# Kernel optimization log

Measured on AMD Instinct MI355X. Metric: run time of the kernel, lower is better.

The kernel has to match this reference:

```python
import jax, jax.numpy as jnp
import numpy as np

B, S, D = 32, 1, 2048
H, KVH, HD = 16, 4, 128
MAXS = 4096
EPS = 1e-5
NREP = H // KVH  # GQA repeat factor = 4
FF = 4 * D
POS = 4095  # decode position (start_pos)


def setup_inputs() -> dict:
    key = jax.random.key(0)
    ks = jax.random.split(key, 12)
    sc = lambda d: 1.0 / np.sqrt(d)
    # RoPE angles for the current token position, [S, HD//2]
    inv_freq = 1.0 / (10000.0 ** (np.arange(0, HD, 2, dtype=np.float32) / HD))
    ang = (POS + np.arange(S, dtype=np.float32))[:, None] * inv_freq[None, :]
    return {
        "x": jax.random.normal(ks[0], (B, S, D), jnp.float32),
        "cos": jnp.asarray(np.cos(ang), jnp.float32),
        "sin": jnp.asarray(np.sin(ang), jnp.float32),
        "k_cache": jax.random.normal(ks[1], (B, MAXS, KVH, HD), jnp.float32),
        "v_cache": jax.random.normal(ks[2], (B, MAXS, KVH, HD), jnp.float32),
        "w_rms_attn": jnp.ones((D,), jnp.float32),
        "wq": jax.random.normal(ks[3], (D, D), jnp.float32) * sc(D),
        "wk": jax.random.normal(ks[4], (D, KVH * HD), jnp.float32) * sc(D),
        "wv": jax.random.normal(ks[5], (D, KVH * HD), jnp.float32) * sc(D),
        "wo": jax.random.normal(ks[6], (D, D), jnp.float32) * sc(D),
        "w_rms_ffn": jnp.ones((D,), jnp.float32),
        "w1": jax.random.normal(ks[7], (D, FF), jnp.float32) * sc(D),
        "w2": jax.random.normal(ks[8], (D, FF), jnp.float32) * sc(D),
        "w3": jax.random.normal(ks[9], (FF, D), jnp.float32) * sc(FF),
        "start_pos": POS,
    }


def _rmsnorm(x, g):
    return x * g * jax.lax.rsqrt(jnp.mean(x * x, axis=-1, keepdims=True) + EPS)


def _rope(x, cos, sin):
    # x: [B, S, h, HD]; complex rotation on (even, odd) pairs
    xr = x.reshape(*x.shape[:-1], HD // 2, 2)
    x0, x1 = xr[..., 0], xr[..., 1]
    c = cos[None, :, None, :]
    s = sin[None, :, None, :]
    r0 = x0 * c - x1 * s
    r1 = x0 * s + x1 * c
    return jnp.stack([r0, r1], axis=-1).reshape(x.shape)


def reference(x, cos, sin, k_cache, v_cache, w_rms_attn, wq, wk, wv, wo,
              w_rms_ffn, w1, w2, w3, start_pos):
    xa = _rmsnorm(x, w_rms_attn)
    xq = (xa @ wq).reshape(B, S, H, HD)
    xk = (xa @ wk).reshape(B, S, KVH, HD)
    xv = (xa @ wv).reshape(B, S, KVH, HD)
    # Source applies RoPE to K and V (not Q) -- reproduced faithfully.
    xk = _rope(xk, cos, sin)
    xv = _rope(xv, cos, sin)
    kc = jax.lax.dynamic_update_slice(k_cache, xk, (0, start_pos, 0, 0))
    vc = jax.lax.dynamic_update_slice(v_cache, xv, (0, start_pos, 0, 0))
    klen = start_pos + S
    keys = jnp.repeat(kc[:, :klen], NREP, axis=2)   # [B, klen, H, HD]
    vals = jnp.repeat(vc[:, :klen], NREP, axis=2)
    att = jnp.einsum('bqhd,bkhd->bhqk', xq, keys) * (HD ** -0.5)
    att = jax.nn.softmax(att, axis=-1)
    y = jnp.einsum('bhqk,bkhd->bqhd', att, vals).reshape(B, S, D)
    h = x + y @ wo
    xf = _rmsnorm(h, w_rms_ffn)
    return h + (jax.nn.silu(xf @ w1) * (xf @ w2)) @ w3
```

## Files before the change

kernel.cpp:

```cpp
#include <hip/hip_runtime.h>
#include <math.h>

#define BB 32
#define DD 2048
#define NKVH 4
#define HDIM 128
#define MAXS 4096
#define FFD 8192
#define POS 4095
#define EPSV 1e-5f
#define SCALE 0.08838834764831845f
#define ASPLIT 16

#define OFF_QT   0u
#define OFF_KT   65536u
#define OFF_VT   81920u
#define OFF_G1   98304u
#define OFF_G2   360448u
#define ZERO_N   622592u
#define OFF_XAT  622592u
#define OFF_RK   688128u
#define OFF_RV   704512u
#define OFF_PML  720896u
#define OFF_PACC 737280u
#define OFF_YT   1785856u
#define OFF_H    1851392u
#define OFF_XFT  1916928u

#define REP32(M) M(0) M(1) M(2) M(3) M(4) M(5) M(6) M(7) M(8) M(9) M(10) M(11) M(12) M(13) M(14) M(15) M(16) M(17) M(18) M(19) M(20) M(21) M(22) M(23) M(24) M(25) M(26) M(27) M(28) M(29) M(30) M(31)
#define REP32A(M,X) M(0,X) M(1,X) M(2,X) M(3,X) M(4,X) M(5,X) M(6,X) M(7,X) M(8,X) M(9,X) M(10,X) M(11,X) M(12,X) M(13,X) M(14,X) M(15,X) M(16,X) M(17,X) M(18,X) M(19,X) M(20,X) M(21,X) M(22,X) M(23,X) M(24,X) M(25,X) M(26,X) M(27,X) M(28,X) M(29,X) M(30,X) M(31,X)

#define DECLA(i) float a##i = 0.f;
#define FMA1(i,k) a##i = fmaf(ap[(k)*32 + (i)], w##k, a##i);
#define STORET(i) tl[i] = a##i;
#define ATOMN(i) atomicAdd(C + (size_t)(i)*N + n, a##i);

template<int N, int CH, bool TOUT>
__device__ __forceinline__ void gemv_body(const float* __restrict__ At,
                                          const float* __restrict__ W,
                                          float* __restrict__ C, int colblk,
                                          float* tile) {
    int tid = (int)threadIdx.x;
    int n = colblk * 256 + tid;
    int d0 = blockIdx.y * CH;
    const float* Wp = W + (size_t)d0 * N + n;
    const float* ap = At + (size_t)d0 * 32;
    REP32(DECLA)
#pragma unroll 4
    for (int dd = 0; dd < CH; dd += 4) {
        float w0 = Wp[0];
        float w1 = Wp[(size_t)N];
        float w2 = Wp[(size_t)N * 2];
        float w3 = Wp[(size_t)N * 3];
        REP32A(FMA1, 0)
        REP32A(FMA1, 1)
        REP32A(FMA1, 2)
        REP32A(FMA1, 3)
        Wp += (size_t)N * 4;
        ap += 128;
    }
    if constexpr (TOUT) {
        float* tl = tile + tid * 33;
        REP32(STORET)
        __syncthreads();
        float* cb = C + (size_t)colblk * 256 * 32;
#pragma unroll
        for (int i = 0; i < 32; ++i) {
            int f = i * 256 + tid;
            atomicAdd(cb + f, tile[(f >> 5) * 33 + (f & 31)]);
        }
    } else {
        REP32(ATOMN)
    }
}

template<int N, int CH, bool TOUT>
__global__ __launch_bounds__(256) void gemv32_kernel(const float* __restrict__ At,
                                                     const float* __restrict__ W,
                                                     float* __restrict__ C) {
    if constexpr (TOUT) {
        __shared__ float tile[256 * 33];
        gemv_body<N, CH, true>(At, W, C, blockIdx.x, tile);
    } else {
        gemv_body<N, CH, false>(At, W, C, blockIdx.x, nullptr);
    }
}

template<int N, int CH, int HALF>
__global__ __launch_bounds__(256) void gemv32_dual_kernel(const float* __restrict__ At,
        const float* __restrict__ W0, const float* __restrict__ W1,
        float* __restrict__ C0, float* __restrict__ C1) {
    __shared__ float tile[256 * 33];
    int bx = blockIdx.x;
    if (bx < HALF) gemv_body<N, CH, true>(At, W0, C0, bx, tile);
    else           gemv_body<N, CH, true>(At, W1, C1, bx - HALF, tile);
}

__global__ void zero_kernel(float* __restrict__ p) {
    p[blockIdx.x * 256 + threadIdx.x] = 0.f;
}

__global__ void rmsnorm_kernel(const float* __restrict__ in, const float* __restrict__ g,
                               float* __restrict__ outT, float* __restrict__ cpy) {
    int b = blockIdx.x;
    int tid = threadIdx.x;
    const float* row = in + b * DD;
    float v[8];
    float ss = 0.f;
#pragma unroll
    for (int i = 0; i < 8; ++i) { v[i] = row[tid + i * 256]; ss += v[i] * v[i]; }
#pragma unroll
    for (int off = 32; off; off >>= 1) ss += __shfl_xor(ss, off);
    __shared__ float red[4];
    if ((tid & 63) == 0) red[tid >> 6] = ss;
    __syncthreads();
    ss = red[0] + red[1] + red[2] + red[3];
    float scale = rsqrtf(ss * (1.f / DD) + EPSV);
#pragma unroll
    for (int i = 0; i < 8; ++i) {
        int idx = tid + i * 256;
        outT[(size_t)idx * 32 + b] = v[i] * g[idx] * scale;
        if (cpy) cpy[b * DD + idx] = v[i];
    }
}

__global__ void rope_kernel(const float* __restrict__ kT, const float* __restrict__ vT,
                            const float* __restrict__ cosb, const float* __restrict__ sinb,
                            float* __restrict__ rk, float* __restrict__ rv) {
    int idx = blockIdx.x * 256 + threadIdx.x;
    int b = idx >> 8, rem = idx & 255;
    int kvh = rem >> 6, i = rem & 63;
    float c = cosb[i], s = sinb[i];
    int col = kvh * HDIM + 2 * i;
    float k0 = kT[(size_t)col * 32 + b], k1 = kT[(size_t)(col + 1) * 32 + b];
    float v0 = vT[(size_t)col * 32 + b], v1 = vT[(size_t)(col + 1) * 32 + b];
    int o = (b * NKVH + kvh) * HDIM + 2 * i;
    rk[o] = k0 * c - k1 * s; rk[o + 1] = k0 * s + k1 * c;
    rv[o] = v0 * c - v1 * s; rv[o + 1] = v0 * s + v1 * c;
}

__global__ __launch_bounds__(256) void attn_partial_kernel(
    const float* __restrict__ qT, const float* __restrict__ kc, const float* __restrict__ vc,
    const float* __restrict__ rk, const float* __restrict__ rv,
    float* __restrict__ pml, float* __restrict__ pacc) {
    int bid = blockIdx.x;
    int split = bid & 15, kvh = (bid >> 4) & 3, b = bid >> 6;
    int tid = threadIdx.x;
    __shared__ float q_s[4][HDIM];
    __shared__ float p_s[4][256];
    __shared__ float red[8][4][HDIM];
    for (int i = tid; i < 4 * HDIM; i += 256)
        q_s[i >> 7][i & 127] = qT[(size_t)(kvh * 512 + i) * 32 + b];
    __syncthreads();
    int t0 = split * 256;
    {
        int t = t0 + tid;
        const float* krow = (t == POS) ? rk + (b * NKVH + kvh) * HDIM
                                       : kc + ((size_t)(b * MAXS + t) * NKVH + kvh) * HDIM;
        float s0 = 0, s1 = 0, s2 = 0, s3 = 0;
#pragma unroll 8
        for (int j = 0; j < HDIM; j += 4) {
            float4 kk = *(const float4*)(krow + j);
            s0 += kk.x * q_s[0][j] + kk.y * q_s[0][j + 1] + kk.z * q_s[0][j + 2] + kk.w * q_s[0][j + 3];
            s1 += kk.x * q_s[1][j] + kk.y * q_s[1][j + 1] + kk.z * q_s[1][j + 2] + kk.w * q_s[1][j + 3];
            s2 += kk.x * q_s[2][j] + kk.y * q_s[2][j + 1] + kk.z * q_s[2][j + 2] + kk.w * q_s[2][j + 3];
            s3 += kk.x * q_s[3][j] + kk.y * q_s[3][j + 1] + kk.z * q_s[3][j + 2] + kk.w * q_s[3][j + 3];
        }
        p_s[0][tid] = s0 * SCALE; p_s[1][tid] = s1 * SCALE;
        p_s[2][tid] = s2 * SCALE; p_s[3][tid] = s3 * SCALE;
    }
    __syncthreads();
    {
        int w = tid >> 6, lane = tid & 63;
        float e0 = p_s[w][lane], e1 = p_s[w][lane + 64];
        float e2 = p_s[w][lane + 128], e3 = p_s[w][lane + 192];
        float m = fmaxf(fmaxf(e0, e1), fmaxf(e2, e3));
#pragma unroll
        for (int off = 32; off; off >>= 1) m = fmaxf(m, __shfl_xor(m, off));
        e0 = __expf(e0 - m); e1 = __expf(e1 - m);
        e2 = __expf(e2 - m); e3 = __expf(e3 - m);
        p_s[w][lane] = e0; p_s[w][lane + 64] = e1;
        p_s[w][lane + 128] = e2; p_s[w][lane + 192] = e3;
        float l = e0 + e1 + e2 + e3;
#pragma unroll
        for (int off = 32; off; off >>= 1) l += __shfl_xor(l, off);
        if (lane == 0) {
            int idx = ((b * NKVH + kvh) * ASPLIT + split) * 4 + w;
            pml[2 * idx] = m; pml[2 * idx + 1] = l;
        }
    }
    __syncthreads();
    {
        int tsub = tid >> 5, q4 = tid & 31;
        int tb = t0 + tsub * 32;
        const float* vbase = vc + ((size_t)(b * MAXS + tb) * NKVH + kvh) * HDIM + q4 * 4;
        float4 a0 = {0, 0, 0, 0}, a1 = a0, a2 = a0, a3 = a0;
        int jmax = (split == ASPLIT - 1 && tsub == 7) ? 31 : 32;
#pragma unroll 4
        for (int j = 0; j < jmax; ++j) {
            float4 vv = *(const float4*)(vbase + (size_t)j * (NKVH * HDIM));
            int tl = tsub * 32 + j;
            float p0 = p_s[0][tl], p1 = p_s[1][tl], p2 = p_s[2][tl], p3 = p_s[3][tl];
            a0.x = fmaf(p0, vv.x, a0.x); a0.y = fmaf(p0, vv.y, a0.y); a0.z = fmaf(p0, vv.z, a0.z); a0.w = fmaf(p0, vv.w, a0.w);
            a1.x = fmaf(p1, vv.x, a1.x); a1.y = fmaf(p1, vv.y, a1.y); a1.z = fmaf(p1, vv.z, a1.z); a1.w = fmaf(p1, vv.w, a1.w);
            a2.x = fmaf(p2, vv.x, a2.x); a2.y = fmaf(p2, vv.y, a2.y); a2.z = fmaf(p2, vv.z, a2.z); a2.w = fmaf(p2, vv.w, a2.w);
            a3.x = fmaf(p3, vv.x, a3.x); a3.y = fmaf(p3, vv.y, a3.y); a3.z = fmaf(p3, vv.z, a3.z); a3.w = fmaf(p3, vv.w, a3.w);
        }
        if (split == ASPLIT - 1 && tsub == 7) {
            float4 vv = *(const float4*)(rv + (b * NKVH + kvh) * HDIM + q4 * 4);
            float p0 = p_s[0][255], p1 = p_s[1][255], p2 = p_s[2][255], p3 = p_s[3][255];
            a0.x = fmaf(p0, vv.x, a0.x); a0.y = fmaf(p0, vv.y, a0.y); a0.z = fmaf(p0, vv.z, a0.z); a0.w = fmaf(p0, vv.w, a0.w);
            a1.x = fmaf(p1, vv.x, a1.x); a1.y = fmaf(p1, vv.y, a1.y); a1.z = fmaf(p1, vv.z, a1.z); a1.w = fmaf(p1, vv.w, a1.w);
            a2.x = fmaf(p2, vv.x, a2.x); a2.y = fmaf(p2, vv.y, a2.y); a2.z = fmaf(p2, vv.z, a2.z); a2.w = fmaf(p2, vv.w, a2.w);
            a3.x = fmaf(p3, vv.x, a3.x); a3.y = fmaf(p3, vv.y, a3.y); a3.z = fmaf(p3, vv.z, a3.z); a3.w = fmaf(p3, vv.w, a3.w);
        }
        *(float4*)&red[tsub][0][q4 * 4] = a0;
        *(float4*)&red[tsub][1][q4 * 4] = a1;
        *(float4*)&red[tsub][2][q4 * 4] = a2;
        *(float4*)&red[tsub][3][q4 * 4] = a3;
    }
    __syncthreads();
    if (tid < 128) {
        int h = tid >> 5, qq = tid & 31;
        float4 s = {0, 0, 0, 0};
#pragma unroll
        for (int r = 0; r < 8; ++r) {
            float4 t4 = *(const float4*)&red[r][h][qq * 4];
            s.x += t4.x; s.y += t4.y; s.z += t4.z; s.w += t4.w;
        }
        int idx = ((b * NKVH + kvh) * ASPLIT + split) * 4 + h;
        *(float4*)(pacc + (size_t)idx * HDIM + qq * 4) = s;
    }
}

__global__ void attn_combine_kernel(const float* __restrict__ pml,
                                    const float* __restrict__ pacc, float* __restrict__ yT) {
    int bid = blockIdx.x;
    int b = bid >> 4, h = bid & 15;
    int kvh = h >> 2, hl = h & 3;
    int d = threadIdx.x;
    float M = -INFINITY;
#pragma unroll
    for (int s = 0; s < ASPLIT; ++s) {
        int idx = ((b * NKVH + kvh) * ASPLIT + s) * 4 + hl;
        M = fmaxf(M, pml[2 * idx]);
    }
    float denom = 0.f, acc = 0.f;
#pragma unroll
    for (int s = 0; s < ASPLIT; ++s) {
        int idx = ((b * NKVH + kvh) * ASPLIT + s) * 4 + hl;
        float e = __expf(pml[2 * idx] - M);
        denom += pml[2 * idx + 1] * e;
        acc += e * pacc[(size_t)idx * HDIM + d];
    }
    yT[(size_t)(h * HDIM + d) * 32 + b] = acc / denom;
}

__global__ void silu_mul_kernel(float* __restrict__ g1, const float* __restrict__ g2) {
    int i = blockIdx.x * 256 + threadIdx.x;
    float a = g1[i], bb = g2[i];
    g1[i] = a * bb / (1.f + __expf(-a));
}

extern "C" void kernel_launch(void* const* d_in, const int* in_sizes, int n_in,
                              void* d_out, int out_size, void* d_ws, size_t ws_size,
                              hipStream_t stream) {
    (void)in_sizes; (void)n_in; (void)out_size; (void)ws_size;
    const float* x    = (const float*)d_in[0];
    const float* cosb = (const float*)d_in[1];
    const float* sinb = (const float*)d_in[2];
    const float* kc   = (const float*)d_in[3];
    const float* vc   = (const float*)d_in[4];
    const float* wra  = (const float*)d_in[5];
    const float* wq   = (const float*)d_in[6];
    const float* wk   = (const float*)d_in[7];
    const float* wv   = (const float*)d_in[8];
    const float* wo   = (const float*)d_in[9];
    const float* wrf  = (const float*)d_in[10];
    const float* w1   = (const float*)d_in[11];
    const float* w2   = (const float*)d_in[12];
    const float* w3   = (const float*)d_in[13];
    float* out = (float*)d_out;
    float* ws  = (float*)d_ws;

    float* qT   = ws + OFF_QT;
    float* kT   = ws + OFF_KT;
    float* vT   = ws + OFF_VT;
    float* g1T  = ws + OFF_G1;
    float* g2T  = ws + OFF_G2;
    float* xaT  = ws + OFF_XAT;
    float* rk   = ws + OFF_RK;
    float* rv   = ws + OFF_RV;
    float* pml  = ws + OFF_PML;
    float* pacc = ws + OFF_PACC;
    float* yT   = ws + OFF_YT;
    float* h    = ws + OFF_H;
    float* xfT  = ws + OFF_XFT;

    zero_kernel<<<ZERO_N / 256, 256, 0, stream>>>(ws);

    rmsnorm_kernel<<<32, 256, 0, stream>>>(x, wra, xaT, h);
    gemv32_kernel<2048, 32, true><<<dim3(8, 64), 256, 0, stream>>>(xaT, wq, qT);
    gemv32_dual_kernel<512, 32, 2><<<dim3(4, 64), 256, 0, stream>>>(xaT, wk, wv, kT, vT);
    rope_kernel<<<32, 256, 0, stream>>>(kT, vT, cosb, sinb, rk, rv);
    attn_partial_kernel<<<2048, 256, 0, stream>>>(qT, kc, vc, rk, rv, pml, pacc);
    attn_combine_kernel<<<512, 128, 0, stream>>>(pml, pacc, yT);
    gemv32_kernel<2048, 32, false><<<dim3(8, 64), 256, 0, stream>>>(yT, wo, h);
    rmsnorm_kernel<<<32, 256, 0, stream>>>(h, wrf, xfT, out);
    gemv32_dual_kernel<8192, 128, 32><<<dim3(64, 16), 256, 0, stream>>>(xfT, w1, w2, g1T, g2T);
    silu_mul_kernel<<<1024, 256, 0, stream>>>(g1T, g2T);
    gemv32_kernel<2048, 128, false><<<dim3(8, 64), 256, 0, stream>>>(g1T, w3, out);
}
```

Baseline: 296.7 us.

## Restructure attention partial so each block covers all KV heads with coalesced rows

The attention partial kernel now assigns one block per (batch, 128-position split) covering all four KV heads. Each thread holds a float4 slice of the query in registers and reads contiguous 4 KB K/V rows, so the whole wavefront issues fully coalesced loads instead of per-thread strided row walks. QK dot products are reduced with cross-lane shuffles, and the partial-result layout and combine kernel are reindexed for 32 splits. The cost is five shuffle rounds per position and a larger partial buffer to combine.

```diff
diff --git a/kernel.cpp b/kernel.cpp
--- a/kernel.cpp
+++ b/kernel.cpp
@@ -10,7 +10,8 @@
 #define POS 4095
 #define EPSV 1e-5f
 #define SCALE 0.08838834764831845f
-#define ASPLIT 16
+#define ASPLIT 32
+#define SPOS 128
 
 #define OFF_QT   0u
 #define OFF_KT   65536u
@@ -22,10 +23,10 @@
 #define OFF_RK   688128u
 #define OFF_RV   704512u
 #define OFF_PML  720896u
-#define OFF_PACC 737280u
-#define OFF_YT   1785856u
-#define OFF_H    1851392u
-#define OFF_XFT  1916928u
+#define OFF_PACC 753664u
+#define OFF_YT   2850816u
+#define OFF_H    2916352u
+#define OFF_XFT  2981888u
 
 #define REP32(M) M(0) M(1) M(2) M(3) M(4) M(5) M(6) M(7) M(8) M(9) M(10) M(11) M(12) M(13) M(14) M(15) M(16) M(17) M(18) M(19) M(20) M(21) M(22) M(23) M(24) M(25) M(26) M(27) M(28) M(29) M(30) M(31)
 #define REP32A(M,X) M(0,X) M(1,X) M(2,X) M(3,X) M(4,X) M(5,X) M(6,X) M(7,X) M(8,X) M(9,X) M(10,X) M(11,X) M(12,X) M(13,X) M(14,X) M(15,X) M(16,X) M(17,X) M(18,X) M(19,X) M(20,X) M(21,X) M(22,X) M(23,X) M(24,X) M(25,X) M(26,X) M(27,X) M(28,X) M(29,X) M(30,X) M(31,X)
@@ -144,92 +145,125 @@
     const float* __restrict__ rk, const float* __restrict__ rv,
     float* __restrict__ pml, float* __restrict__ pacc) {
     int bid = blockIdx.x;
-    int split = bid & 15, kvh = (bid >> 4) & 3, b = bid >> 6;
+    int split = bid & 31, b = bid >> 5;
     int tid = threadIdx.x;
-    __shared__ float q_s[4][HDIM];
-    __shared__ float p_s[4][256];
-    __shared__ float red[8][4][HDIM];
-    for (int i = tid; i < 4 * HDIM; i += 256)
-        q_s[i >> 7][i & 127] = qT[(size_t)(kvh * 512 + i) * 32 + b];
+    int kvh = (tid >> 5) & 3;
+    int c = tid & 31;
+    int hi = tid >> 7;
+    __shared__ float p_s[16][SPOS];
+    __shared__ float red[128][17];
+
+    float4 q4[4];
+#pragma unroll
+    for (int h = 0; h < 4; ++h) {
+        int col = (kvh * 4 + h) * HDIM + c * 4;
+        q4[h].x = qT[(size_t)(col + 0) * 32 + b];
+        q4[h].y = qT[(size_t)(col + 1) * 32 + b];
+        q4[h].z = qT[(size_t)(col + 2) * 32 + b];
+        q4[h].w = qT[(size_t)(col + 3) * 32 + b];
+    }
+    int t0 = split * SPOS;
+    const float* kbase = kc + (size_t)(b * MAXS + t0) * (NKVH * HDIM);
+    const float* vbase = vc + (size_t)(b * MAXS + t0) * (NKVH * HDIM);
+
+#define QK_BODY(SRC, POSL)                                                      \
+    {                                                                           \
+        float4 kk = *(const float4*)(SRC);                                      \
+        float r0 = kk.x * q4[0].x + kk.y * q4[0].y + kk.z * q4[0].z + kk.w * q4[0].w; \
+        float r1 = kk.x * q4[1].x + kk.y * q4[1].y + kk.z * q4[1].z + kk.w * q4[1].w; \
+        float r2 = kk.x * q4[2].x + kk.y * q4[2].y + kk.z * q4[2].z + kk.w * q4[2].w; \
+        float r3 = kk.x * q4[3].x + kk.y * q4[3].y + kk.z * q4[3].z + kk.w * q4[3].w; \
+        _Pragma("unroll")                                                       \
+        for (int m = 1; m < 32; m <<= 1) {                                      \
+            r0 += __shfl_xor(r0, m); r1 += __shfl_xor(r1, m);                   \
+            r2 += __shfl_xor(r2, m); r3 += __shfl_xor(r3, m);                   \
+        }                                                                       \
+        if (c == 0) {                                                           \
+            p_s[kvh * 4 + 0][POSL] = r0 * SCALE;                                \
+            p_s[kvh * 4 + 1][POSL] = r1 * SCALE;                                \
+            p_s[kvh * 4 + 2][POSL] = r2 * SCALE;                                \
+            p_s[kvh * 4 + 3][POSL] = r3 * SCALE;                                \
+        }                                                                       \
+    }
+
+#pragma unroll 8
+    for (int iter = 0; iter < 63; ++iter) {
+        QK_BODY(kbase + iter * 1024 + tid * 4, iter * 2 + hi)
+    }
+    {
+        int posl = 126 + hi;
+        const float* src = (t0 + posl == POS)
+            ? rk + (size_t)(b * NKVH + kvh) * HDIM + c * 4
+            : kbase + 63 * 1024 + tid * 4;
+        QK_BODY(src, posl)
+    }
     __syncthreads();
-    int t0 = split * 256;
-    {
-        int t = t0 + tid;
-        const float* krow = (t == POS) ? rk + (b * NKVH + kvh) * HDIM
-                                       : kc + ((size_t)(b * MAXS + t) * NKVH + kvh) * HDIM;
-        float s0 = 0, s1 = 0, s2 = 0, s3 = 0;
-#pragma unroll 8
-        for (int j = 0; j < HDIM; j += 4) {
-            float4 kk = *(const float4*)(krow + j);
-            s0 += kk.x * q_s[0][j] + kk.y * q_s[0][j + 1] + kk.z * q_s[0][j + 2] + kk.w * q_s[0][j + 3];
-            s1 += kk.x * q_s[1][j] + kk.y * q_s[1][j + 1] + kk.z * q_s[1][j + 2] + kk.w * q_s[1][j + 3];
-            s2 += kk.x * q_s[2][j] + kk.y * q_s[2][j + 1] + kk.z * q_s[2][j + 2] + kk.w * q_s[2][j + 3];
-            s3 += kk.x * q_s[3][j] + kk.y * q_s[3][j + 1] + kk.z * q_s[3][j + 2] + kk.w * q_s[3][j + 3];
-        }
-        p_s[0][tid] = s0 * SCALE; p_s[1][tid] = s1 * SCALE;
-        p_s[2][tid] = s2 * SCALE; p_s[3][tid] = s3 * SCALE;
-    }
-    __syncthreads();
+
     {
         int w = tid >> 6, lane = tid & 63;
-        float e0 = p_s[w][lane], e1 = p_s[w][lane + 64];
-        float e2 = p_s[w][lane + 128], e3 = p_s[w][lane + 192];
-        float m = fmaxf(fmaxf(e0, e1), fmaxf(e2, e3));
-#pragma unroll
-        for (int off = 32; off; off >>= 1) m = fmaxf(m, __shfl_xor(m, off));
-        e0 = __expf(e0 - m); e1 = __expf(e1 - m);
-        e2 = __expf(e2 - m); e3 = __expf(e3 - m);
-        p_s[w][lane] = e0; p_s[w][lane + 64] = e1;
-        p_s[w][lane + 128] = e2; p_s[w][lane + 192] = e3;
-        float l = e0 + e1 + e2 + e3;
-#pragma unroll
-        for (int off = 32; off; off >>= 1) l += __shfl_xor(l, off);
-        if (lane == 0) {
-            int idx = ((b * NKVH + kvh) * ASPLIT + split) * 4 + w;
-            pml[2 * idx] = m; pml[2 * idx + 1] = l;
+#pragma unroll
+        for (int hh = 0; hh < 4; ++hh) {
+            int h = w * 4 + hh;
+            float e0 = p_s[h][lane], e1 = p_s[h][lane + 64];
+            float m = fmaxf(e0, e1);
+#pragma unroll
+            for (int off = 32; off; off >>= 1) m = fmaxf(m, __shfl_xor(m, off));
+            e0 = __expf(e0 - m); e1 = __expf(e1 - m);
+            p_s[h][lane] = e0; p_s[h][lane + 64] = e1;
+            float l = e0 + e1;
+#pragma unroll
+            for (int off = 32; off; off >>= 1) l += __shfl_xor(l, off);
+            if (lane == 0) {
+                int idx = ((b * ASPLIT + split) * 16 + h) * 2;
+                pml[idx] = m; pml[idx + 1] = l;
+            }
         }
     }
     __syncthreads();
+
+    float4 a0 = {0, 0, 0, 0}, a1 = a0, a2 = a0, a3 = a0;
+#define PV_BODY(SRC, POSL)                                                      \
+    {                                                                           \
+        float4 vv = *(const float4*)(SRC);                                      \
+        float p0 = p_s[kvh * 4 + 0][POSL], p1 = p_s[kvh * 4 + 1][POSL];         \
+        float p2 = p_s[kvh * 4 + 2][POSL], p3 = p_s[kvh * 4 + 3][POSL];         \
+        a0.x = fmaf(p0, vv.x, a0.x); a0.y = fmaf(p0, vv.y, a0.y);               \
+        a0.z = fmaf(p0, vv.z, a0.z); a0.w = fmaf(p0, vv.w, a0.w);               \
+        a1.x = fmaf(p1, vv.x, a1.x); a1.y = fmaf(p1, vv.y, a1.y);               \
+        a1.z = fmaf(p1, vv.z, a1.z); a1.w = fmaf(p1, vv.w, a1.w);               \
+        a2.x = fmaf(p2, vv.x, a2.x); a2.y = fmaf(p2, vv.y, a2.y);               \
+        a2.z = fmaf(p2, vv.z, a2.z); a2.w = fmaf(p2, vv.w, a2.w);               \
+        a3.x = fmaf(p3, vv.x, a3.x); a3.y = fmaf(p3, vv.y, a3.y);               \
+        a3.z = fmaf(p3, vv.z, a3.z); a3.w = fmaf(p3, vv.w, a3.w);               \
+    }
+#pragma unroll 8
+    for (int iter = 0; iter < 63; ++iter) {
+        PV_BODY(vbase + iter * 1024 + tid * 4, iter * 2 + hi)
+    }
     {
-        int tsub = tid >> 5, q4 = tid & 31;
-        int tb = t0 + tsub * 32;
-        const float* vbase = vc + ((size_t)(b * MAXS + tb) * NKVH + kvh) * HDIM + q4 * 4;
-        float4 a0 = {0, 0, 0, 0}, a1 = a0, a2 = a0, a3 = a0;
-        int jmax = (split == ASPLIT - 1 && tsub == 7) ? 31 : 32;
-#pragma unroll 4
-        for (int j = 0; j < jmax; ++j) {
-            float4 vv = *(const float4*)(vbase + (size_t)j * (NKVH * HDIM));
-            int tl = tsub * 32 + j;
-            float p0 = p_s[0][tl], p1 = p_s[1][tl], p2 = p_s[2][tl], p3 = p_s[3][tl];
-            a0.x = fmaf(p0, vv.x, a0.x); a0.y = fmaf(p0, vv.y, a0.y); a0.z = fmaf(p0, vv.z, a0.z); a0.w = fmaf(p0, vv.w, a0.w);
-            a1.x = fmaf(p1, vv.x, a1.x); a1.y = fmaf(p1, vv.y, a1.y); a1.z = fmaf(p1, vv.z, a1.z); a1.w = fmaf(p1, vv.w, a1.w);
-            a2.x = fmaf(p2, vv.x, a2.x); a2.y = fmaf(p2, vv.y, a2.y); a2.z = fmaf(p2, vv.z, a2.z); a2.w = fmaf(p2, vv.w, a2.w);
-            a3.x = fmaf(p3, vv.x, a3.x); a3.y = fmaf(p3, vv.y, a3.y); a3.z = fmaf(p3, vv.z, a3.z); a3.w = fmaf(p3, vv.w, a3.w);
-        }
-        if (split == ASPLIT - 1 && tsub == 7) {
-            float4 vv = *(const float4*)(rv + (b * NKVH + kvh) * HDIM + q4 * 4);
-            float p0 = p_s[0][255], p1 = p_s[1][255], p2 = p_s[2][255], p3 = p_s[3][255];
-            a0.x = fmaf(p0, vv.x, a0.x); a0.y = fmaf(p0, vv.y, a0.y); a0.z = fmaf(p0, vv.z, a0.z); a0.w = fmaf(p0, vv.w, a0.w);
-            a1.x = fmaf(p1, vv.x, a1.x); a1.y = fmaf(p1, vv.y, a1.y); a1.z = fmaf(p1, vv.z, a1.z); a1.w = fmaf(p1, vv.w, a1.w);
-            a2.x = fmaf(p2, vv.x, a2.x); a2.y = fmaf(p2, vv.y, a2.y); a2.z = fmaf(p2, vv.z, a2.z); a2.w = fmaf(p2, vv.w, a2.w);
-            a3.x = fmaf(p3, vv.x, a3.x); a3.y = fmaf(p3, vv.y, a3.y); a3.z = fmaf(p3, vv.z, a3.z); a3.w = fmaf(p3, vv.w, a3.w);
-        }
-        *(float4*)&red[tsub][0][q4 * 4] = a0;
-        *(float4*)&red[tsub][1][q4 * 4] = a1;
-        *(float4*)&red[tsub][2][q4 * 4] = a2;
-        *(float4*)&red[tsub][3][q4 * 4] = a3;
+        int posl = 126 + hi;
+        const float* src = (t0 + posl == POS)
+            ? rv + (size_t)(b * NKVH + kvh) * HDIM + c * 4
+            : vbase + 63 * 1024 + tid * 4;
+        PV_BODY(src, posl)
+    }
+    if (tid >= 128) {
+        float* r = &red[tid - 128][0];
+        *(float4*)(r + 0) = a0; *(float4*)(r + 4) = a1;
+        *(float4*)(r + 8) = a2; *(float4*)(r + 12) = a3;
     }
     __syncthreads();
     if (tid < 128) {
-        int h = tid >> 5, qq = tid & 31;
-        float4 s = {0, 0, 0, 0};
-#pragma unroll
-        for (int r = 0; r < 8; ++r) {
-            float4 t4 = *(const float4*)&red[r][h][qq * 4];
-            s.x += t4.x; s.y += t4.y; s.z += t4.z; s.w += t4.w;
-        }
-        int idx = ((b * NKVH + kvh) * ASPLIT + split) * 4 + h;
-        *(float4*)(pacc + (size_t)idx * HDIM + qq * 4) = s;
+        const float* r = &red[tid][0];
+        a0.x += r[0];  a0.y += r[1];  a0.z += r[2];  a0.w += r[3];
+        a1.x += r[4];  a1.y += r[5];  a1.z += r[6];  a1.w += r[7];
+        a2.x += r[8];  a2.y += r[9];  a2.z += r[10]; a2.w += r[11];
+        a3.x += r[12]; a3.y += r[13]; a3.z += r[14]; a3.w += r[15];
+        size_t base = ((size_t)(b * ASPLIT + split) * 16 + kvh * 4) * HDIM + c * 4;
+        *(float4*)(pacc + base + 0 * HDIM) = a0;
+        *(float4*)(pacc + base + 1 * HDIM) = a1;
+        *(float4*)(pacc + base + 2 * HDIM) = a2;
+        *(float4*)(pacc + base + 3 * HDIM) = a3;
     }
 }
 
@@ -237,20 +271,17 @@
                                     const float* __restrict__ pacc, float* __restrict__ yT) {
     int bid = blockIdx.x;
     int b = bid >> 4, h = bid & 15;
-    int kvh = h >> 2, hl = h & 3;
     int d = threadIdx.x;
     float M = -INFINITY;
-#pragma unroll
+#pragma unroll 8
+    for (int s = 0; s < ASPLIT; ++s)
+        M = fmaxf(M, pml[((b * ASPLIT + s) * 16 + h) * 2]);
+    float denom = 0.f, acc = 0.f;
+#pragma unroll 4
     for (int s = 0; s < ASPLIT; ++s) {
-        int idx = ((b * NKVH + kvh) * ASPLIT + s) * 4 + hl;
-        M = fmaxf(M, pml[2 * idx]);
-    }
-    float denom = 0.f, acc = 0.f;
-#pragma unroll
-    for (int s = 0; s < ASPLIT; ++s) {
-        int idx = ((b * NKVH + kvh) * ASPLIT + s) * 4 + hl;
-        float e = __expf(pml[2 * idx] - M);
-        denom += pml[2 * idx + 1] * e;
+        int idx = (b * ASPLIT + s) * 16 + h;
+        float e = __expf(pml[idx * 2] - M);
+        denom += pml[idx * 2 + 1] * e;
         acc += e * pacc[(size_t)idx * HDIM + d];
     }
     yT[(size_t)(h * HDIM + d) * 32 + b] = acc / denom;
@@ -303,7 +334,7 @@
     gemv32_kernel<2048, 32, true><<<dim3(8, 64), 256, 0, stream>>>(xaT, wq, qT);
     gemv32_dual_kernel<512, 32, 2><<<dim3(4, 64), 256, 0, stream>>>(xaT, wk, wv, kT, vT);
     rope_kernel<<<32, 256, 0, stream>>>(kT, vT, cosb, sinb, rk, rv);
-    attn_partial_kernel<<<2048, 256, 0, stream>>>(qT, kc, vc, rk, rv, pml, pacc);
+    attn_partial_kernel<<<1024, 256, 0, stream>>>(qT, kc, vc, rk, rv, pml, pacc);
     attn_combine_kernel<<<512, 128, 0, stream>>>(pml, pacc, yT);
     gemv32_kernel<2048, 32, false><<<dim3(8, 64), 256, 0, stream>>>(yT, wo, h);
     rmsnorm_kernel<<<32, 256, 0, stream>>>(h, wrf, xfT, out);
```

Measured after the change: 337.1 us. +13.6%, slower.
